# Kernel optimization log

Measured on AMD Instinct MI355X. Metric: run time of the kernel, lower is better.

The kernel has to match this reference:

```python
import jax, jax.numpy as jnp
import numpy as np


def setup_inputs() -> dict:
    key = jax.random.key(0)
    k1, k2 = jax.random.split(key, 2)
    N, H, W, FIN = 64, 64, 64, 64
    FH, FW, FOUT = 4, 4, 128
    L = (H // FH) * (W // FW)  # 256 output locations (stride == kernel)
    X = jax.random.normal(k1, (N, H, W, FIN), dtype=jnp.float32)
    # 'alexnet' init: normal(0, 0.01), unshared per-location filters
    filters = 0.01 * jax.random.normal(k2, (1, L, FH, FW, FIN, FOUT), dtype=jnp.float32)
    bias = jnp.zeros((FOUT,), dtype=jnp.float32)  # bias init value 0.0
    return {"X": X, "filters": filters, "bias": bias}


def reference(X, filters, bias):
    N, H, W, C = X.shape
    _, L, fh, fw, fin, fout = filters.shape
    rows, cols = H // fh, W // fw
    # image_to_patches (stride==kernel branch): non-overlapping patch extraction
    # patches[n, r*cols+c, i, j, ch] = X[n, r*fh+i, c*fw+j, ch]
    patches = X.reshape(N, rows, fh, cols, fw, C)
    patches = patches.transpose(0, 1, 3, 2, 4, 5).reshape(N, L, fh, fw, C)
    # broadcast-multiply + reduce_sum over (fh, fw, fin) == per-location GEMM
    Z = jnp.einsum('nlijc,lijcf->nlf', patches, filters[0]) + bias
    Z = Z.reshape(N, rows, cols, fout)
    return jax.nn.relu(Z)
```

## Files before the change

kernel.cpp:

```cpp
#include <hip/hip_runtime.h>


typedef __bf16 bf16x8 __attribute__((ext_vector_type(8)));
typedef float f32x4 __attribute__((ext_vector_type(4)));

__device__ __forceinline__ unsigned pack2(float a, float b) {
  __bf16 lo = (__bf16)a, hi = (__bf16)b;
  return (unsigned)__builtin_bit_cast(unsigned short, lo) |
         ((unsigned)__builtin_bit_cast(unsigned short, hi) << 16);
}

__global__ __launch_bounds__(512, 4) void bioconv_blk(
    const float* __restrict__ X, const float* __restrict__ Fw,
    const float* __restrict__ bias, float* __restrict__ out) {
  const int bx = blockIdx.x;
  const int xcd = bx & 7;
  const int idx = bx >> 3;
  const int l = xcd * 32 + (idx >> 1);
  const int fh = idx & 1;
  const int r = l >> 4, c = l & 15;

  const int t = threadIdx.x;
  const int wave = t >> 6, lane = t & 63;
  const int q = lane >> 4, nl = lane & 15;
  const int m0 = (wave >> 1) * 16;
  const int n0 = (wave & 1) * 32;

  __shared__ __align__(16) unsigned short As[2][64 * 128];
  __shared__ __align__(16) unsigned Bs[2][64 * 68];

  const int arow = t >> 3;
  const int alane = t & 7;
  const float* gA = X + (size_t)arow * 262144 + r * 16384 + c * 256;
  const float* gB = Fw + (size_t)l * 131072 + fh * 64 + (size_t)arow * 256;

  float4 vA[4], vB[4];

  auto loadA = [&](int s) {
    const float* g = gA + (s >> 1) * 4096 + (s & 1) * 128;
#pragma unroll
    for (int rep = 0; rep < 4; ++rep)
      vA[rep] = *(const float4*)(g + (alane + rep * 8) * 4);
  };
  auto loadB = [&](int s) {
    const float* g = gB + s * 16384;
#pragma unroll
    for (int rep = 0; rep < 2; ++rep) {
      vB[rep * 2] = *(const float4*)(g + (alane + rep * 8) * 4);
      vB[rep * 2 + 1] = *(const float4*)(g + 128 + (alane + rep * 8) * 4);
    }
  };
  auto writeA = [&](int buf) {
    unsigned* base = (unsigned*)&As[buf][0];
#pragma unroll
    for (int rep = 0; rep < 4; ++rep) {
      const int f4 = alane + rep * 8;
      uint2 u;
      u.x = pack2(vA[rep].x, vA[rep].y);
      u.y = pack2(vA[rep].z, vA[rep].w);
      *(uint2*)(base + arow * 64 + ((f4 * 2) ^ ((arow & 7) << 2))) = u;
    }
  };
  auto writeB = [&](int buf) {
    unsigned* base = (unsigned*)&Bs[buf][0];
#pragma unroll
    for (int rep = 0; rep < 2; ++rep) {
      const int f4 = alane + rep * 8;
      uint4 v;
      v.x = pack2(vB[rep * 2].x, vB[rep * 2 + 1].x);
      v.y = pack2(vB[rep * 2].y, vB[rep * 2 + 1].y);
      v.z = pack2(vB[rep * 2].z, vB[rep * 2 + 1].z);
      v.w = pack2(vB[rep * 2].w, vB[rep * 2 + 1].w);
      *(uint4*)(base + arow * 68 + f4 * 4) = v;
    }
  };

  f32x4 acc[2];
  acc[0] = (f32x4){0.f, 0.f, 0.f, 0.f};
  acc[1] = (f32x4){0.f, 0.f, 0.f, 0.f};

  auto compute = [&](int buf) {
#pragma unroll
    for (int kk = 0; kk < 4; ++kk) {
      const unsigned short* ap =
          &As[buf][(m0 + nl) * 128 + ((kk * 32 + q * 8) ^ ((nl & 7) << 3))];
      bf16x8 af = *(const bf16x8*)ap;
#pragma unroll
      for (int fb = 0; fb < 2; ++fb) {
        const unsigned* bp =
            (const unsigned*)&Bs[buf][0] + (kk * 16 + q * 4) * 68 + n0 + fb * 16 + nl;
        uint4 v;
        v.x = bp[0];
        v.y = bp[68];
        v.z = bp[136];
        v.w = bp[204];
        bf16x8 bfr = __builtin_bit_cast(bf16x8, v);
        acc[fb] = __builtin_amdgcn_mfma_f32_16x16x32_bf16(af, bfr, acc[fb], 0, 0, 0);
      }
    }
  };

  loadA(0);
  loadB(0);
  writeA(0);
  writeB(0);
  loadA(1);
  loadB(1);
#pragma unroll
  for (int s = 0; s < 8; ++s) {
    __syncthreads();
    compute(s & 1);
    if (s + 1 < 8) {
      writeA((s + 1) & 1);
      writeB((s + 1) & 1);
    }
    if (s + 2 < 8) {
      loadA(s + 2);
      loadB(s + 2);
    }
  }

#pragma unroll
  for (int fb = 0; fb < 2; ++fb) {
    const int f = fh * 64 + n0 + fb * 16 + nl;
    const float bv = bias[f];
    float* ob = out + (size_t)l * 128 + f;
#pragma unroll
    for (int v = 0; v < 4; ++v) {
      const int row = m0 + q * 4 + v;
      ob[(size_t)row * 32768] = fmaxf(acc[fb][v] + bv, 0.f);
    }
  }
}

extern "C" void kernel_launch(void* const* d_in, const int* in_sizes, int n_in,
                              void* d_out, int out_size, void* d_ws, size_t ws_size,
                              hipStream_t stream) {
  const float* X = (const float*)d_in[0];
  const float* Fw = (const float*)d_in[1];
  const float* bias = (const float*)d_in[2];
  float* out = (float*)d_out;
  bioconv_blk<<<512, 512, 0, stream>>>(X, Fw, bias, out);
}
```

Baseline: 238.9 us.

## Compute all 128 output channels per block, halving grid and sharing the X tile

Each block now handles one location with all 128 output filters instead of splitting filters across two blocks, so each X patch is loaded and converted once rather than twice. The grid drops from 512 to 256 blocks, each wave doing four MFMA tiles. The load mappings are reworked (float2 loads of A per wave across batch rows, B padded to a 140-word stride), and __syncthreads is replaced by a manual lgkmcnt wait plus s_barrier with a sched_barrier. The cost is half as many blocks to fill the GPU, more registers and LDS per block, and the occupancy hint removed from launch bounds.

```diff
diff --git a/kernel.cpp b/kernel.cpp
--- a/kernel.cpp
+++ b/kernel.cpp
@@ -3,6 +3,8 @@
 
 typedef __bf16 bf16x8 __attribute__((ext_vector_type(8)));
 typedef float f32x4 __attribute__((ext_vector_type(4)));
+
+#define SBP 140
 
 __device__ __forceinline__ unsigned pack2(float a, float b) {
   __bf16 lo = (__bf16)a, hi = (__bf16)b;
@@ -10,74 +12,70 @@
          ((unsigned)__builtin_bit_cast(unsigned short, hi) << 16);
 }
 
-__global__ __launch_bounds__(512, 4) void bioconv_blk(
+__global__ __launch_bounds__(512) void bioconv_full(
     const float* __restrict__ X, const float* __restrict__ Fw,
     const float* __restrict__ bias, float* __restrict__ out) {
   const int bx = blockIdx.x;
-  const int xcd = bx & 7;
-  const int idx = bx >> 3;
-  const int l = xcd * 32 + (idx >> 1);
-  const int fh = idx & 1;
+  const int l = (bx & 7) * 32 + (bx >> 3);
   const int r = l >> 4, c = l & 15;
 
   const int t = threadIdx.x;
   const int wave = t >> 6, lane = t & 63;
   const int q = lane >> 4, nl = lane & 15;
   const int m0 = (wave >> 1) * 16;
-  const int n0 = (wave & 1) * 32;
+  const int n0 = (wave & 1) * 64;
 
   __shared__ __align__(16) unsigned short As[2][64 * 128];
-  __shared__ __align__(16) unsigned Bs[2][64 * 68];
+  __shared__ __align__(16) unsigned Bs[2][64 * SBP];
 
-  const int arow = t >> 3;
-  const int alane = t & 7;
-  const float* gA = X + (size_t)arow * 262144 + r * 16384 + c * 256;
-  const float* gB = Fw + (size_t)l * 131072 + fh * 64 + (size_t)arow * 256;
+  const float* gA = X + r * 16384 + c * 256;
+  const float* gB = Fw + (size_t)l * 131072;
 
-  float4 vA[4], vB[4];
+  float2 vA[8];
+  float4 vB0[4], vB1[4];
 
   auto loadA = [&](int s) {
-    const float* g = gA + (s >> 1) * 4096 + (s & 1) * 128;
+    const int off = (s >> 1) * 4096 + (s & 1) * 128 + 2 * lane;
 #pragma unroll
-    for (int rep = 0; rep < 4; ++rep)
-      vA[rep] = *(const float4*)(g + (alane + rep * 8) * 4);
+    for (int m = 0; m < 8; ++m) {
+      const int n = m * 8 + wave;
+      vA[m] = *(const float2*)(gA + (size_t)n * 262144 + off);
+    }
   };
   auto loadB = [&](int s) {
-    const float* g = gB + s * 16384;
+    const float* base = gB + s * 16384 + 4 * (lane & 31);
 #pragma unroll
-    for (int rep = 0; rep < 2; ++rep) {
-      vB[rep * 2] = *(const float4*)(g + (alane + rep * 8) * 4);
-      vB[rep * 2 + 1] = *(const float4*)(g + 128 + (alane + rep * 8) * 4);
+    for (int m = 0; m < 4; ++m) {
+      const int kp = wave * 8 + m * 2 + (lane >> 5);
+      vB0[m] = *(const float4*)(base + kp * 256);
+      vB1[m] = *(const float4*)(base + kp * 256 + 128);
     }
   };
   auto writeA = [&](int buf) {
     unsigned* base = (unsigned*)&As[buf][0];
 #pragma unroll
-    for (int rep = 0; rep < 4; ++rep) {
-      const int f4 = alane + rep * 8;
-      uint2 u;
-      u.x = pack2(vA[rep].x, vA[rep].y);
-      u.y = pack2(vA[rep].z, vA[rep].w);
-      *(uint2*)(base + arow * 64 + ((f4 * 2) ^ ((arow & 7) << 2))) = u;
+    for (int m = 0; m < 8; ++m) {
+      const int n = m * 8 + wave;
+      base[n * 64 + (lane ^ ((n & 7) << 2))] = pack2(vA[m].x, vA[m].y);
     }
   };
   auto writeB = [&](int buf) {
-    unsigned* base = (unsigned*)&Bs[buf][0];
+    unsigned* bw = (unsigned*)&Bs[buf][0] + 4 * (lane & 31);
 #pragma unroll
-    for (int rep = 0; rep < 2; ++rep) {
-      const int f4 = alane + rep * 8;
+    for (int m = 0; m < 4; ++m) {
+      const int kp = wave * 8 + m * 2 + (lane >> 5);
       uint4 v;
-      v.x = pack2(vB[rep * 2].x, vB[rep * 2 + 1].x);
-      v.y = pack2(vB[rep * 2].y, vB[rep * 2 + 1].y);
-      v.z = pack2(vB[rep * 2].z, vB[rep * 2 + 1].z);
-      v.w = pack2(vB[rep * 2].w, vB[rep * 2 + 1].w);
-      *(uint4*)(base + arow * 68 + f4 * 4) = v;
+      v.x = pack2(vB0[m].x, vB1[m].x);
+      v.y = pack2(vB0[m].y, vB1[m].y);
+      v.z = pack2(vB0[m].z, vB1[m].z);
+      v.w = pack2(vB0[m].w, vB1[m].w);
+      *(uint4*)(bw + kp * SBP) = v;
     }
   };
 
-  f32x4 acc[2];
-  acc[0] = (f32x4){0.f, 0.f, 0.f, 0.f};
-  acc[1] = (f32x4){0.f, 0.f, 0.f, 0.f};
+  f32x4 acc[4];
+#pragma unroll
+  for (int fb = 0; fb < 4; ++fb) acc[fb] = (f32x4){0.f, 0.f, 0.f, 0.f};
 
   auto compute = [&](int buf) {
 #pragma unroll
@@ -85,15 +83,15 @@
       const unsigned short* ap =
           &As[buf][(m0 + nl) * 128 + ((kk * 32 + q * 8) ^ ((nl & 7) << 3))];
       bf16x8 af = *(const bf16x8*)ap;
+      const unsigned* bp = (const unsigned*)&Bs[buf][0] + (kk * 16 + q * 4) * SBP + n0 + nl;
 #pragma unroll
-      for (int fb = 0; fb < 2; ++fb) {
-        const unsigned* bp =
-            (const unsigned*)&Bs[buf][0] + (kk * 16 + q * 4) * 68 + n0 + fb * 16 + nl;
+      for (int fb = 0; fb < 4; ++fb) {
+        const unsigned* b = bp + fb * 16;
         uint4 v;
-        v.x = bp[0];
-        v.y = bp[68];
-        v.z = bp[136];
-        v.w = bp[204];
+        v.x = b[0];
+        v.y = b[SBP];
+        v.z = b[2 * SBP];
+        v.w = b[3 * SBP];
         bf16x8 bfr = __builtin_bit_cast(bf16x8, v);
         acc[fb] = __builtin_amdgcn_mfma_f32_16x16x32_bf16(af, bfr, acc[fb], 0, 0, 0);
       }
@@ -108,7 +106,9 @@
   loadB(1);
 #pragma unroll
   for (int s = 0; s < 8; ++s) {
-    __syncthreads();
+    asm volatile("s_waitcnt lgkmcnt(0)" ::: "memory");
+    __builtin_amdgcn_s_barrier();
+    __builtin_amdgcn_sched_barrier(0);
     compute(s & 1);
     if (s + 1 < 8) {
       writeA((s + 1) & 1);
@@ -121,8 +121,8 @@
   }
 
 #pragma unroll
-  for (int fb = 0; fb < 2; ++fb) {
-    const int f = fh * 64 + n0 + fb * 16 + nl;
+  for (int fb = 0; fb < 4; ++fb) {
+    const int f = n0 + fb * 16 + nl;
     const float bv = bias[f];
     float* ob = out + (size_t)l * 128 + f;
 #pragma unroll
@@ -140,5 +140,5 @@
   const float* Fw = (const float*)d_in[1];
   const float* bias = (const float*)d_in[2];
   float* out = (float*)d_out;
-  bioconv_blk<<<512, 512, 0, stream>>>(X, Fw, bias, out);
+  bioconv_full<<<256, 512, 0, stream>>>(X, Fw, bias, out);
 }
```

Measured after the change: 241.9 us. About the same (+1.2%).
